# Kernel tuning notes

Hardware: AMD Instinct MI355X
Metric: run time of the kernel (lower is better)

The kernel has to match this reference:

```python
import jax, jax.numpy as jnp
import numpy as np

NUM_GRAPHS = 1024  # static number of segments for global_mean_pool


def setup_inputs() -> dict:
    key = jax.random.key(0)
    ks = jax.random.split(key, 16)
    N, E, F_IN, H = 100000, 1000000, 32, 64
    NUM_ATOM, NUM_ACT, L = 16, 8, 3
    s = 0.05
    x = jax.random.normal(ks[0], (N, F_IN), dtype=jnp.float32)
    edge_index = jax.random.randint(ks[1], (2, E), 0, N, dtype=jnp.int64)
    batch = jnp.sort(jax.random.randint(ks[2], (N,), 0, NUM_GRAPHS, dtype=jnp.int64))
    W_emb = jax.random.normal(ks[3], (F_IN, H), dtype=jnp.float32) * s
    b_emb = jnp.zeros((H,), dtype=jnp.float32)
    W_convs = jax.random.normal(ks[4], (L, H, H), dtype=jnp.float32) * s
    b_convs = jnp.zeros((L, H), dtype=jnp.float32)
    W_act = jax.random.normal(ks[5], (H, NUM_ACT), dtype=jnp.float32) * s
    b_act = jnp.zeros((NUM_ACT,), dtype=jnp.float32)
    W_tgt = jax.random.normal(ks[6], (H, 1), dtype=jnp.float32) * s
    b_tgt = jnp.zeros((1,), dtype=jnp.float32)
    W_atom = jax.random.normal(ks[7], (H, NUM_ATOM), dtype=jnp.float32) * s
    b_atom = jnp.zeros((NUM_ATOM,), dtype=jnp.float32)
    return {"x": x, "edge_index": edge_index, "batch": batch,
            "W_emb": W_emb, "b_emb": b_emb, "W_convs": W_convs, "b_convs": b_convs,
            "W_act": W_act, "b_act": b_act, "W_tgt": W_tgt, "b_tgt": b_tgt,
            "W_atom": W_atom, "b_atom": b_atom}


def reference(x, edge_index, batch, W_emb, b_emb, W_convs, b_convs,
              W_act, b_act, W_tgt, b_tgt, W_atom, b_atom):
    N = x.shape[0]
    # --- GCN normalization with self-loops (PyG GCNConv default) ---
    self_idx = jnp.arange(N, dtype=edge_index.dtype)
    src = jnp.concatenate([edge_index[0], self_idx])  # message source (row)
    dst = jnp.concatenate([edge_index[1], self_idx])  # aggregation target (col)
    ones_e = jnp.ones(src.shape[0], dtype=x.dtype)
    deg = jax.ops.segment_sum(ones_e, dst, num_segments=N)  # in-degree + self-loop
    dinv = jnp.where(deg > 0, jax.lax.rsqrt(deg), 0.0)
    norm = (dinv[src] * dinv[dst])[:, None]  # [E+N, 1]

    h = jax.nn.relu(x @ W_emb + b_emb)  # node embedding
    for i in range(W_convs.shape[0]):
        m = (h @ W_convs[i])[src] * norm            # gather + scale
        agg = jax.ops.segment_sum(m, dst, num_segments=N)  # scatter-add
        h = jax.nn.relu(agg + b_convs[i])

    # --- global mean pool over graphs ---
    cnt = jax.ops.segment_sum(jnp.ones(N, dtype=x.dtype), batch, num_segments=NUM_GRAPHS)
    pooled = jax.ops.segment_sum(h, batch, num_segments=NUM_GRAPHS)
    pooled = pooled / jnp.maximum(cnt, 1.0)[:, None]

    action_type_logits = pooled @ W_act + b_act            # [G, num_action_types]
    target_node_logits = (h @ W_tgt + b_tgt)[:, 0]         # [N]
    new_atom_type_logits = pooled @ W_atom + b_atom        # [G, num_atom_types]
    return (action_type_logits, target_node_logits, new_atom_type_logits, h)
```

## Files before the change

### kernel.cpp

```cpp
#include <hip/hip_runtime.h>
#include <hip/hip_fp16.h>

#define HD 64
#define FIN 32
#define NG 1024
#define STRIDE 64
#define SLOT0 4
#define DEGCAP 59
#define SH 72

#define BINW 128
#define NBMAX 1024
#define EPB 2048
#define BINCAP 2048

typedef _Float16 f16x8 __attribute__((ext_vector_type(8)));
typedef float f32x4 __attribute__((ext_vector_type(4)));
typedef int i32x4 __attribute__((ext_vector_type(4)));

__device__ __forceinline__ int fmap(int jt, int c) {
    return (jt < 2) ? (2 * c + jt) : (32 + 2 * c + (jt - 2));
}

__global__ __launch_bounds__(256) void k_prep(const int* __restrict__ dst,
                                              int* __restrict__ blkHist,
                                              int E, int NBINS,
                                              __half2* __restrict__ BaZR,
                                              __half2* __restrict__ BbZR,
                                              const float* __restrict__ Wconv,
                                              __half* __restrict__ Wf, int wtotal,
                                              const float* __restrict__ Wemb,
                                              __half* __restrict__ Wef) {
    __shared__ int hist[NBMAX];
    int b = blockIdx.x, t = threadIdx.x;
    if (b < 48) {
        int tid = b * 256 + t;
        if (tid < wtotal) {
            int layer = tid >> 12;
            int r = tid & 4095;
            int frag = r >> 9, lane = (r >> 3) & 63, e = r & 7;
            int jt = frag >> 1, kh = frag & 1;
            int k = kh * 32 + (lane >> 4) * 8 + e;
            int n = fmap(jt, lane & 15);
            Wf[tid] = (_Float16)Wconv[(size_t)layer * 4096 + k * 64 + n];
        }
    } else if (b < 56) {
        int tid = (b - 48) * 256 + t;
        if (tid < 2048) {
            int jt = tid >> 9, lane = (tid >> 3) & 63, e = tid & 7;
            int k = (lane >> 4) * 8 + e;
            int n = fmap(jt, lane & 15);
            Wef[tid] = (_Float16)Wemb[k * HD + n];
        }
    } else if (b == 56) {
        __half2 z = __floats2half2_rn(0.f, 0.f);
        if (t < 32) BaZR[t] = z;
        else if (t < 64) BbZR[t - 32] = z;
    }
    int e0 = b * EPB;
    if (e0 < E) {
        for (int i = t; i < NBMAX; i += 256) hist[i] = 0;
        __syncthreads();
        int e1 = e0 + EPB; if (e1 > E) e1 = E;
        for (int e = e0 + t; e < e1; e += 256) atomicAdd(&hist[dst[e] >> 7], 1);
        __syncthreads();
        for (int i = t; i < NBINS; i += 256) blkHist[b * NBMAX + i] = hist[i];
    }
}

__global__ __launch_bounds__(512) void k_scanA(int* __restrict__ blkHist,
                                               int* __restrict__ binTot, int nb) {
    __shared__ int s[512];
    int i = blockIdx.x;
    int t = threadIdx.x;
    int x = (t < nb) ? blkHist[t * NBMAX + i] : 0;
    s[t] = x;
    __syncthreads();
    for (int off = 1; off < 512; off <<= 1) {
        int v = s[t];
        int u = (t >= off) ? s[t - off] : 0;
        __syncthreads();
        s[t] = v + u;
        __syncthreads();
    }
    if (t < nb) blkHist[t * NBMAX + i] = s[t] - x;
    if (t == 511) binTot[i] = s[511];
}

__global__ __launch_bounds__(256) void k_scatter(const int* __restrict__ src,
                                                 const int* __restrict__ dst,
                                                 const int* __restrict__ blkBase,
                                                 int* __restrict__ binned,
                                                 int E, int NBINS) {
    __shared__ int base[NBMAX];
    __shared__ int lpos[NBMAX];
    int b = blockIdx.x, t = threadIdx.x;
    for (int i = t; i < NBMAX; i += 256) {
        lpos[i] = 0;
        base[i] = (i < NBINS) ? blkBase[b * NBMAX + i] : 0;
    }
    __syncthreads();
    int e0 = b * EPB;
    int e1 = e0 + EPB; if (e1 > E) e1 = E;
    for (int e = e0 + t; e < e1; e += 256) {
        int d = dst[e];
        int bin = d >> 7;
        int off = base[bin] + atomicAdd(&lpos[bin], 1);
        if (off < BINCAP)
            binned[bin * BINCAP + off] = (src[e] << 7) | (d & (BINW - 1));
    }
}

__global__ __launch_bounds__(256) void k_csr(const int* __restrict__ binned,
                                             const int* __restrict__ binTot,
                                             int* __restrict__ col, int N) {
    __shared__ int img[BINW * 64];
    __shared__ int cnt[BINW];
    int b = blockIdx.x, t = threadIdx.x;
    for (int i = t; i < BINW; i += 256) cnt[i] = 0;
    __syncthreads();
    int s = b * BINCAP;
    int tot = binTot[b]; if (tot > BINCAP) tot = BINCAP;
    int e = s + tot;
    for (int i = s + t; i < e; i += 256) {
        int w = binned[i];
        int ld = w & (BINW - 1);
        int p = atomicAdd(&cnt[ld], 1);
        if (p < STRIDE - SLOT0) img[ld * 64 + SLOT0 + p] = (int)((unsigned)w >> 7);
    }
    __syncthreads();
    for (int i = t; i < BINW; i += 256) img[i * 64] = cnt[i];
    __syncthreads();
    int v0 = b * BINW;
    int* out = col + ((size_t)v0 << 6);
    for (int j = t; j < BINW * 16; j += 256) {
        int row = j >> 4, j16 = j & 15;
        int node = v0 + row;
        int deg = cnt[row]; if (deg > DEGCAP) deg = DEGCAP;
        bool keep = (j16 == 0) || (j16 <= ((deg + 3) >> 2));
        if (node < N && keep)
            *(i32x4*)(out + j * 4) = *(i32x4*)&img[j * 4];
    }
}

__device__ __forceinline__ void gemm_from_lds(const __half* hs, const float* dvs,
                                              const float4* __restrict__ Wf4,
                                              __half2* __restrict__ Bout,
                                              int node0, int N, int t) {
    int lane = t & 63;
    int wv = t >> 6;
    int lm = lane & 15, kq = lane >> 4;
    union U { float4 f; f16x8 h; };
    U a0, a1;
    const __half* hrow = hs + (size_t)(wv * 16 + lm) * SH;
    a0.f = *(const float4*)(hrow + kq * 8);
    a1.f = *(const float4*)(hrow + 32 + kq * 8);
    f32x4 acc[4];
#pragma unroll
    for (int jt = 0; jt < 4; jt++) acc[jt] = (f32x4){0.f, 0.f, 0.f, 0.f};
#pragma unroll
    for (int jt = 0; jt < 4; jt++) {
        U b0, b1;
        b0.f = Wf4[(jt * 2 + 0) * 64 + lane];
        b1.f = Wf4[(jt * 2 + 1) * 64 + lane];
        acc[jt] = __builtin_amdgcn_mfma_f32_16x16x32_f16(a0.h, b0.h, acc[jt], 0, 0, 0);
        acc[jt] = __builtin_amdgcn_mfma_f32_16x16x32_f16(a1.h, b1.h, acc[jt], 0, 0, 0);
    }
#pragma unroll
    for (int r = 0; r < 4; r++) {
        int lv = wv * 16 + kq * 4 + r;
        int v = node0 + lv;
        if (v < N) {
            float dv = dvs[lv];
            *(Bout + (size_t)v * 32 + lm) = __floats2half2_rn(acc[0][r] * dv, acc[1][r] * dv);
            *(Bout + (size_t)v * 32 + 16 + lm) = __floats2half2_rn(acc[2][r] * dv, acc[3][r] * dv);
        }
    }
}

__global__ __launch_bounds__(256) void k_emb_gemm0(const float* __restrict__ x,
                                                   const float4* __restrict__ Wef4,
                                                   const float* __restrict__ bemb,
                                                   const int* __restrict__ col,
                                                   const float4* __restrict__ Wf0,
                                                   __half2* __restrict__ Bout, int N) {
    __shared__ __half hs[64 * SH];
    __shared__ float dvs[64];
    int t = threadIdx.x;
    int lane = t & 63;
    int wv = t >> 6;
    int node0 = blockIdx.x * 64;
    int nodew = node0 + wv * 16;
    int m = lane & 15, kq = lane >> 4;

    int vm = nodew + m;
    if (vm > N - 1) vm = N - 1;
    const float4* xr = (const float4*)(x + (size_t)vm * FIN + kq * 8);
    float4 xa = xr[0], xb = xr[1];
    f16x8 a;
    a[0] = (_Float16)xa.x; a[1] = (_Float16)xa.y; a[2] = (_Float16)xa.z; a[3] = (_Float16)xa.w;
    a[4] = (_Float16)xb.x; a[5] = (_Float16)xb.y; a[6] = (_Float16)xb.z; a[7] = (_Float16)xb.w;

    union U { float4 f; f16x8 h; };
    f32x4 acc[4];
#pragma unroll
    for (int jt = 0; jt < 4; jt++) {
        U b; b.f = Wef4[jt * 64 + lane];
        acc[jt] = (f32x4){0.f, 0.f, 0.f, 0.f};
        acc[jt] = __builtin_amdgcn_mfma_f32_16x16x32_f16(a, b.h, acc[jt], 0, 0, 0);
    }
    float b01x = bemb[2 * m], b01y = bemb[2 * m + 1];
    float b23x = bemb[32 + 2 * m], b23y = bemb[32 + 2 * m + 1];
    __half2 z = __floats2half2_rn(0.f, 0.f);
#pragma unroll
    for (int r = 0; r < 4; r++) {
        int lv = wv * 16 + kq * 4 + r;
        int v = node0 + lv;
        __half2 p01 = z, p23 = z;
        if (v < N) {
            p01 = __floats2half2_rn(fmaxf(acc[0][r] + b01x, 0.f),
                                    fmaxf(acc[1][r] + b01y, 0.f));
            p23 = __floats2half2_rn(fmaxf(acc[2][r] + b23x, 0.f),
                                    fmaxf(acc[3][r] + b23y, 0.f));
        }
        *(__half2*)(hs + (size_t)lv * SH + 2 * m) = p01;
        *(__half2*)(hs + (size_t)lv * SH + 32 + 2 * m) = p23;
        if (m == 0)
            dvs[lv] = (v < N) ? rsqrtf((float)(col[(size_t)v << 6] + 1)) : 1.f;
    }
    __syncthreads();
    gemm_from_lds(hs, dvs, Wf0, Bout, node0, N, t);
}

__global__ __launch_bounds__(256) void k_layer(const __half2* __restrict__ Bin,
                                               const int* __restrict__ col,
                                               const float* __restrict__ bias,
                                               const float4* __restrict__ Wnext,
                                               __half2* __restrict__ Bout,
                                               int N, int ZR) {
    __shared__ __half hs[64 * SH];
    __shared__ float dvs[64];
    int t = threadIdx.x;
    int lane = t & 63;
    int wv = t >> 6;
    int node0 = blockIdx.x * 64;
    int q = lane >> 4, p = lane & 15;
    float4 b4 = *(const float4*)(bias + 4 * p);

#pragma unroll
    for (int pass = 0; pass < 4; pass++) {
        int lv = wv * 16 + pass * 4 + q;
        int v = node0 + lv;
        int vc = (v < N) ? v : 0;
        const int* bucket = col + ((size_t)vc << 6);
        int degraw = bucket[0];
        int deg = degraw > DEGCAP ? DEGCAP : degraw;
        int rounds = (deg + 4) >> 2;

        float2 a0 = make_float2(0.f, 0.f), a1 = make_float2(0.f, 0.f);
        for (int rd = 0; rd < rounds; rd++) {
            int4 iq = *(const int4*)(bucket + SLOT0 + rd * 4);
            int idx[4] = {iq.x, iq.y, iq.z, iq.w};
#pragma unroll
            for (int r = 0; r < 4; r++) {
                int i = rd * 4 + r;
                idx[r] = (i < deg) ? idx[r] : ((i == deg) ? vc : ZR);
            }
            float2 raw[4];
#pragma unroll
            for (int r = 0; r < 4; r++)
                raw[r] = *(const float2*)(Bin + (size_t)idx[r] * 32 + p * 2);
#pragma unroll
            for (int r = 0; r < 4; r++) {
                float2 f0 = __half22float2(((const __half2*)&raw[r])[0]);
                float2 f1 = __half22float2(((const __half2*)&raw[r])[1]);
                a0.x += f0.x; a0.y += f0.y; a1.x += f1.x; a1.y += f1.y;
            }
        }
        float dv = rsqrtf((float)(degraw + 1));
        float r0 = fmaxf(dv * a0.x + b4.x, 0.f);
        float r1 = fmaxf(dv * a0.y + b4.y, 0.f);
        float r2 = fmaxf(dv * a1.x + b4.z, 0.f);
        float r3 = fmaxf(dv * a1.y + b4.w, 0.f);
        if (v >= N) { r0 = r1 = r2 = r3 = 0.f; dv = 1.f; }
        __half* hrow = hs + (size_t)lv * SH + 4 * p;
        *(__half2*)(hrow) = __floats2half2_rn(r0, r1);
        *(__half2*)(hrow + 2) = __floats2half2_rn(r2, r3);
        if (p == 0) dvs[lv] = dv;
    }
    __syncthreads();
    gemm_from_lds(hs, dvs, Wnext, Bout, node0, N, t);
}

__global__ __launch_bounds__(256) void k_gather_last(const __half2* __restrict__ Bin,
                                                     const int* __restrict__ col,
                                                     const float* __restrict__ bias,
                                                     float* __restrict__ hout,
                                                     const float* __restrict__ Wtgt,
                                                     const float* __restrict__ btgt,
                                                     float* __restrict__ tgt,
                                                     int N, int ZR) {
    int t = threadIdx.x;
    int lane = t & 63;
    int wv = t >> 6;
    int q = lane >> 4, p = lane & 15;
    int v = blockIdx.x * 16 + wv * 4 + q;
    if (v >= N) return;

    const int* bucket = col + ((size_t)v << 6);
    int degraw = bucket[0];
    int deg = degraw > DEGCAP ? DEGCAP : degraw;
    int rounds = (deg + 4) >> 2;

    float2 a0 = make_float2(0.f, 0.f), a1 = make_float2(0.f, 0.f);
    for (int rd = 0; rd < rounds; rd++) {
        int4 iq = *(const int4*)(bucket + SLOT0 + rd * 4);
        int idx[4] = {iq.x, iq.y, iq.z, iq.w};
#pragma unroll
        for (int r = 0; r < 4; r++) {
            int i = rd * 4 + r;
            idx[r] = (i < deg) ? idx[r] : ((i == deg) ? v : ZR);
        }
        float2 raw[4];
#pragma unroll
        for (int r = 0; r < 4; r++)
            raw[r] = *(const float2*)(Bin + (size_t)idx[r] * 32 + p * 2);
#pragma unroll
        for (int r = 0; r < 4; r++) {
            float2 f0 = __half22float2(((const __half2*)&raw[r])[0]);
            float2 f1 = __half22float2(((const __half2*)&raw[r])[1]);
            a0.x += f0.x; a0.y += f0.y; a1.x += f1.x; a1.y += f1.y;
        }
    }
    float dv = rsqrtf((float)(degraw + 1));
    float4 b4 = *(const float4*)(bias + 4 * p);
    float r0 = fmaxf(dv * a0.x + b4.x, 0.f);
    float r1 = fmaxf(dv * a0.y + b4.y, 0.f);
    float r2 = fmaxf(dv * a1.x + b4.z, 0.f);
    float r3 = fmaxf(dv * a1.y + b4.w, 0.f);
    *(f32x4*)(hout + (size_t)v * HD + 4 * p) = (f32x4){r0, r1, r2, r3};
    float4 w4 = *(const float4*)(Wtgt + 4 * p);
    float pp = r0 * w4.x + r1 * w4.y + r2 * w4.z + r3 * w4.w;
    pp += __shfl_xor(pp, 1, 64); pp += __shfl_xor(pp, 2, 64);
    pp += __shfl_xor(pp, 4, 64); pp += __shfl_xor(pp, 8, 64);
    if (p == 0) __builtin_nontemporal_store(pp + btgt[0], tgt + v);
}

__global__ __launch_bounds__(256) void k_pool(const float* __restrict__ h,
                                              const int* __restrict__ batch,
                                              const float* __restrict__ Wact,
                                              const float* __restrict__ bact,
                                              const float* __restrict__ Watom,
                                              const float* __restrict__ batom,
                                              float* __restrict__ out_act,
                                              float* __restrict__ out_atom, int N) {
    int g = blockIdx.x;
    int t = threadIdx.x;
    int q = t >> 4, p = t & 15;
    int lo = 0, hi = N;
    while (lo < hi) { int mid = (lo + hi) >> 1; if (batch[mid] < g) lo = mid + 1; else hi = mid; }
    int s = lo;
    hi = N;
    while (lo < hi) { int mid = (lo + hi) >> 1; if (batch[mid] < g + 1) lo = mid + 1; else hi = mid; }
    int e2 = lo;
    float4 acc = make_float4(0.f, 0.f, 0.f, 0.f);
    for (int v = s + q; v < e2; v += 16) {
        float4 c = *(const float4*)(h + (size_t)v * HD + p * 4);
        acc.x += c.x; acc.y += c.y; acc.z += c.z; acc.w += c.w;
    }
    __shared__ float4 part[16][16];
    part[q][p] = acc;
    __syncthreads();
    __shared__ float pl[HD];
    if (t < 16) {
        float4 tot = part[0][t];
#pragma unroll
        for (int k = 1; k < 16; k++) {
            float4 c = part[k][t];
            tot.x += c.x; tot.y += c.y; tot.z += c.z; tot.w += c.w;
        }
        float cnt = fmaxf((float)(e2 - s), 1.f);
        pl[t * 4 + 0] = tot.x / cnt; pl[t * 4 + 1] = tot.y / cnt;
        pl[t * 4 + 2] = tot.z / cnt; pl[t * 4 + 3] = tot.w / cnt;
    }
    __syncthreads();
    if (t < 8) {
        float a = bact[t];
#pragma unroll
        for (int k = 0; k < HD; k++) a += pl[k] * Wact[k * 8 + t];
        out_act[g * 8 + t] = a;
    }
    if (t < 16) {
        float a = batom[t];
#pragma unroll
        for (int k = 0; k < HD; k++) a += pl[k] * Watom[k * 16 + t];
        out_atom[g * 16 + t] = a;
    }
}

extern "C" void kernel_launch(void* const* d_in, const int* in_sizes, int n_in,
                              void* d_out, int out_size, void* d_ws, size_t ws_size,
                              hipStream_t stream) {
    const float* x     = (const float*)d_in[0];
    const int*   ei    = (const int*)d_in[1];
    const int*   batch = (const int*)d_in[2];
    const float* Wemb  = (const float*)d_in[3];
    const float* bemb  = (const float*)d_in[4];
    const float* Wconv = (const float*)d_in[5];
    const float* bconv = (const float*)d_in[6];
    const float* Wact  = (const float*)d_in[7];
    const float* bact  = (const float*)d_in[8];
    const float* Wtgt  = (const float*)d_in[9];
    const float* btgt  = (const float*)d_in[10];
    const float* Watom = (const float*)d_in[11];
    const float* batom = (const float*)d_in[12];

    const int N = in_sizes[0] / FIN;
    const int E = in_sizes[1] / 2;
    const int L = in_sizes[5] / (HD * HD);
    const int Npad = (N + 63) & ~63;
    const int ZR = Npad;

    int*     col = (int*)d_ws;
    __half2* Ba  = (__half2*)(col + ((size_t)N << 6));
    __half2* Bb  = Ba + (size_t)(Npad + 64) * 32;
    __half*  Wf  = (__half*)(Bb + (size_t)(Npad + 64) * 32);
    __half*  Wef = Wf + (size_t)L * 4096;

    int* binned  = (int*)Bb;
    int* blkHist = (int*)((char*)Bb + (8u << 20));
    int* binTot  = (int*)((char*)Bb + (11u << 20));

    const int* srcA = ei;
    const int* dstA = ei + E;

    float* out_act  = (float*)d_out;
    float* out_tgt  = out_act + (size_t)NG * 8;
    float* out_atom = out_tgt + N;
    float* out_h    = out_atom + (size_t)NG * 16;

    const int nbG = (N + 63) / 64;
    const int nbLast = (N + 15) / 16;
    const int wtotal = L * 4096;
    const int nbF1 = (E + EPB - 1) / EPB;
    const int NBINS = (N + BINW - 1) / BINW;
    const int nbPrep = nbF1 > 57 ? nbF1 : 57;

    k_prep<<<nbPrep, 256, 0, stream>>>(dstA, blkHist, E, NBINS,
                                       Ba + (size_t)ZR * 32, Bb + (size_t)ZR * 32,
                                       Wconv, Wf, wtotal, Wemb, Wef);
    k_scanA<<<NBINS, 512, 0, stream>>>(blkHist, binTot, nbF1);
    k_scatter<<<nbF1, 256, 0, stream>>>(srcA, dstA, blkHist, binned, E, NBINS);
    k_csr<<<NBINS, 256, 0, stream>>>(binned, binTot, col, N);
    k_emb_gemm0<<<nbG, 256, 0, stream>>>(x, (const float4*)Wef, bemb, col,
                                         (const float4*)Wf, Ba, N);

    __half2* cur = Ba;
    __half2* nxt = Bb;
    for (int l = 0; l < L - 1; ++l) {
        k_layer<<<nbG, 256, 0, stream>>>(cur, col, bconv + l * HD,
                                         (const float4*)(Wf + (size_t)(l + 1) * 4096),
                                         nxt, N, ZR);
        __half2* tmp = cur; cur = nxt; nxt = tmp;
    }
    k_gather_last<<<nbLast, 256, 0, stream>>>(cur, col, bconv + (size_t)(L - 1) * HD,
                                              out_h, Wtgt, btgt, out_tgt, N, ZR);
    k_pool<<<NG, 256, 0, stream>>>(out_h, batch, Wact, bact, Watom, batom,
                                   out_act, out_atom, N);
}
```

Measured before the change: 224.7 us.

## Fuse global mean-pool accumulation into last gather kernel via atomics

Moves the per-graph sum of final node features into the last gather kernel. Each block accumulates into shared memory per local graph and then does global atomic adds into a pooled buffer that the prep kernel zeroes. The pool kernel becomes a small heads kernel that only divides by the count and applies the two linear heads. This avoids re-reading the 25MB h output, in exchange for extra shared and global atomics and float summation order that is no longer deterministic.

```diff
diff --git a/kernel.cpp b/kernel.cpp
--- a/kernel.cpp
+++ b/kernel.cpp
@@ -30,7 +30,8 @@
                                               const float* __restrict__ Wconv,
                                               __half* __restrict__ Wf, int wtotal,
                                               const float* __restrict__ Wemb,
-                                              __half* __restrict__ Wef) {
+                                              __half* __restrict__ Wef,
+                                              float* __restrict__ pooled) {
     __shared__ int hist[NBMAX];
     int b = blockIdx.x, t = threadIdx.x;
     if (b < 48) {
@@ -56,6 +57,12 @@
         __half2 z = __floats2half2_rn(0.f, 0.f);
         if (t < 32) BaZR[t] = z;
         else if (t < 64) BbZR[t - 32] = z;
+    } else if (b < 61) {
+        f32x4* p4 = (f32x4*)pooled;
+        f32x4 z4 = (f32x4){0.f, 0.f, 0.f, 0.f};
+        int base = (b - 57) * 4096;
+#pragma unroll
+        for (int k = 0; k < 16; k++) p4[base + k * 256 + t] = z4;
     }
     int e0 = b * EPB;
     if (e0 < E) {
@@ -295,58 +302,90 @@
 __global__ __launch_bounds__(256) void k_gather_last(const __half2* __restrict__ Bin,
                                                      const int* __restrict__ col,
                                                      const float* __restrict__ bias,
+                                                     const int* __restrict__ batch,
+                                                     float* __restrict__ pooled,
                                                      float* __restrict__ hout,
                                                      const float* __restrict__ Wtgt,
                                                      const float* __restrict__ btgt,
                                                      float* __restrict__ tgt,
                                                      int N, int ZR) {
+    __shared__ float gsum[16 * HD];
     int t = threadIdx.x;
     int lane = t & 63;
     int wv = t >> 6;
     int q = lane >> 4, p = lane & 15;
-    int v = blockIdx.x * 16 + wv * 4 + q;
-    if (v >= N) return;
-
-    const int* bucket = col + ((size_t)v << 6);
-    int degraw = bucket[0];
-    int deg = degraw > DEGCAP ? DEGCAP : degraw;
-    int rounds = (deg + 4) >> 2;
-
-    float2 a0 = make_float2(0.f, 0.f), a1 = make_float2(0.f, 0.f);
-    for (int rd = 0; rd < rounds; rd++) {
-        int4 iq = *(const int4*)(bucket + SLOT0 + rd * 4);
-        int idx[4] = {iq.x, iq.y, iq.z, iq.w};
-#pragma unroll
-        for (int r = 0; r < 4; r++) {
-            int i = rd * 4 + r;
-            idx[r] = (i < deg) ? idx[r] : ((i == deg) ? v : ZR);
-        }
-        float2 raw[4];
-#pragma unroll
-        for (int r = 0; r < 4; r++)
-            raw[r] = *(const float2*)(Bin + (size_t)idx[r] * 32 + p * 2);
-#pragma unroll
-        for (int r = 0; r < 4; r++) {
-            float2 f0 = __half22float2(((const __half2*)&raw[r])[0]);
-            float2 f1 = __half22float2(((const __half2*)&raw[r])[1]);
-            a0.x += f0.x; a0.y += f0.y; a1.x += f1.x; a1.y += f1.y;
-        }
-    }
-    float dv = rsqrtf((float)(degraw + 1));
-    float4 b4 = *(const float4*)(bias + 4 * p);
-    float r0 = fmaxf(dv * a0.x + b4.x, 0.f);
-    float r1 = fmaxf(dv * a0.y + b4.y, 0.f);
-    float r2 = fmaxf(dv * a1.x + b4.z, 0.f);
-    float r3 = fmaxf(dv * a1.y + b4.w, 0.f);
-    *(f32x4*)(hout + (size_t)v * HD + 4 * p) = (f32x4){r0, r1, r2, r3};
-    float4 w4 = *(const float4*)(Wtgt + 4 * p);
-    float pp = r0 * w4.x + r1 * w4.y + r2 * w4.z + r3 * w4.w;
-    pp += __shfl_xor(pp, 1, 64); pp += __shfl_xor(pp, 2, 64);
-    pp += __shfl_xor(pp, 4, 64); pp += __shfl_xor(pp, 8, 64);
-    if (p == 0) __builtin_nontemporal_store(pp + btgt[0], tgt + v);
-}
-
-__global__ __launch_bounds__(256) void k_pool(const float* __restrict__ h,
+    int v0 = blockIdx.x * 16;
+    int v = v0 + wv * 4 + q;
+#pragma unroll
+    for (int k = 0; k < 4; k++) gsum[k * 256 + t] = 0.f;
+    int g0 = batch[(v0 < N) ? v0 : (N - 1)];
+    __syncthreads();
+
+    if (v < N) {
+        const int* bucket = col + ((size_t)v << 6);
+        int degraw = bucket[0];
+        int deg = degraw > DEGCAP ? DEGCAP : degraw;
+        int rounds = (deg + 4) >> 2;
+
+        float2 a0 = make_float2(0.f, 0.f), a1 = make_float2(0.f, 0.f);
+        for (int rd = 0; rd < rounds; rd++) {
+            int4 iq = *(const int4*)(bucket + SLOT0 + rd * 4);
+            int idx[4] = {iq.x, iq.y, iq.z, iq.w};
+#pragma unroll
+            for (int r = 0; r < 4; r++) {
+                int i = rd * 4 + r;
+                idx[r] = (i < deg) ? idx[r] : ((i == deg) ? v : ZR);
+            }
+            float2 raw[4];
+#pragma unroll
+            for (int r = 0; r < 4; r++)
+                raw[r] = *(const float2*)(Bin + (size_t)idx[r] * 32 + p * 2);
+#pragma unroll
+            for (int r = 0; r < 4; r++) {
+                float2 f0 = __half22float2(((const __half2*)&raw[r])[0]);
+                float2 f1 = __half22float2(((const __half2*)&raw[r])[1]);
+                a0.x += f0.x; a0.y += f0.y; a1.x += f1.x; a1.y += f1.y;
+            }
+        }
+        float dv = rsqrtf((float)(degraw + 1));
+        float4 b4 = *(const float4*)(bias + 4 * p);
+        float r0 = fmaxf(dv * a0.x + b4.x, 0.f);
+        float r1 = fmaxf(dv * a0.y + b4.y, 0.f);
+        float r2 = fmaxf(dv * a1.x + b4.z, 0.f);
+        float r3 = fmaxf(dv * a1.y + b4.w, 0.f);
+        *(f32x4*)(hout + (size_t)v * HD + 4 * p) = (f32x4){r0, r1, r2, r3};
+
+        int lg = batch[v] - g0;
+        if (lg < 16) {
+            atomicAdd(&gsum[lg * HD + 4 * p + 0], r0);
+            atomicAdd(&gsum[lg * HD + 4 * p + 1], r1);
+            atomicAdd(&gsum[lg * HD + 4 * p + 2], r2);
+            atomicAdd(&gsum[lg * HD + 4 * p + 3], r3);
+        } else {
+            atomicAdd(&pooled[(size_t)(g0 + lg) * HD + 4 * p + 0], r0);
+            atomicAdd(&pooled[(size_t)(g0 + lg) * HD + 4 * p + 1], r1);
+            atomicAdd(&pooled[(size_t)(g0 + lg) * HD + 4 * p + 2], r2);
+            atomicAdd(&pooled[(size_t)(g0 + lg) * HD + 4 * p + 3], r3);
+        }
+
+        float4 w4 = *(const float4*)(Wtgt + 4 * p);
+        float pp = r0 * w4.x + r1 * w4.y + r2 * w4.z + r3 * w4.w;
+        pp += __shfl_xor(pp, 1, 64); pp += __shfl_xor(pp, 2, 64);
+        pp += __shfl_xor(pp, 4, 64); pp += __shfl_xor(pp, 8, 64);
+        if (p == 0) __builtin_nontemporal_store(pp + btgt[0], tgt + v);
+    }
+    __syncthreads();
+
+    int vlast = v0 + 15; if (vlast > N - 1) vlast = N - 1;
+    int gspan = (v0 < N) ? (batch[vlast] - g0 + 1) : 0;
+    if (gspan > 16) gspan = 16;
+    for (int c = t; c < gspan * HD; c += 256) {
+        float s = gsum[c];
+        if (s != 0.f) atomicAdd(&pooled[(size_t)(g0 + (c >> 6)) * HD + (c & 63)], s);
+    }
+}
+
+__global__ __launch_bounds__(64) void k_heads(const float* __restrict__ pooled,
                                               const int* __restrict__ batch,
                                               const float* __restrict__ Wact,
                                               const float* __restrict__ bact,
@@ -356,45 +395,26 @@
                                               float* __restrict__ out_atom, int N) {
     int g = blockIdx.x;
     int t = threadIdx.x;
-    int q = t >> 4, p = t & 15;
     int lo = 0, hi = N;
     while (lo < hi) { int mid = (lo + hi) >> 1; if (batch[mid] < g) lo = mid + 1; else hi = mid; }
     int s = lo;
     hi = N;
     while (lo < hi) { int mid = (lo + hi) >> 1; if (batch[mid] < g + 1) lo = mid + 1; else hi = mid; }
-    int e2 = lo;
-    float4 acc = make_float4(0.f, 0.f, 0.f, 0.f);
-    for (int v = s + q; v < e2; v += 16) {
-        float4 c = *(const float4*)(h + (size_t)v * HD + p * 4);
-        acc.x += c.x; acc.y += c.y; acc.z += c.z; acc.w += c.w;
-    }
-    __shared__ float4 part[16][16];
-    part[q][p] = acc;
-    __syncthreads();
+    float cnt = fmaxf((float)(lo - s), 1.f);
     __shared__ float pl[HD];
-    if (t < 16) {
-        float4 tot = part[0][t];
-#pragma unroll
-        for (int k = 1; k < 16; k++) {
-            float4 c = part[k][t];
-            tot.x += c.x; tot.y += c.y; tot.z += c.z; tot.w += c.w;
-        }
-        float cnt = fmaxf((float)(e2 - s), 1.f);
-        pl[t * 4 + 0] = tot.x / cnt; pl[t * 4 + 1] = tot.y / cnt;
-        pl[t * 4 + 2] = tot.z / cnt; pl[t * 4 + 3] = tot.w / cnt;
-    }
+    pl[t] = pooled[(size_t)g * HD + t] / cnt;
     __syncthreads();
     if (t < 8) {
         float a = bact[t];
 #pragma unroll
         for (int k = 0; k < HD; k++) a += pl[k] * Wact[k * 8 + t];
         out_act[g * 8 + t] = a;
-    }
-    if (t < 16) {
-        float a = batom[t];
-#pragma unroll
-        for (int k = 0; k < HD; k++) a += pl[k] * Watom[k * 16 + t];
-        out_atom[g * 16 + t] = a;
+    } else if (t < 24) {
+        int j = t - 8;
+        float a = batom[j];
+#pragma unroll
+        for (int k = 0; k < HD; k++) a += pl[k] * Watom[k * 16 + j];
+        out_atom[g * 16 + j] = a;
     }
 }
 
@@ -426,6 +446,7 @@
     __half2* Bb  = Ba + (size_t)(Npad + 64) * 32;
     __half*  Wf  = (__half*)(Bb + (size_t)(Npad + 64) * 32);
     __half*  Wef = Wf + (size_t)L * 4096;
+    float*   pooled = (float*)(Wef + 2048);
 
     int* binned  = (int*)Bb;
     int* blkHist = (int*)((char*)Bb + (8u << 20));
@@ -444,11 +465,11 @@
     const int wtotal = L * 4096;
     const int nbF1 = (E + EPB - 1) / EPB;
     const int NBINS = (N + BINW - 1) / BINW;
-    const int nbPrep = nbF1 > 57 ? nbF1 : 57;
+    const int nbPrep = nbF1 > 61 ? nbF1 : 61;
 
     k_prep<<<nbPrep, 256, 0, stream>>>(dstA, blkHist, E, NBINS,
                                        Ba + (size_t)ZR * 32, Bb + (size_t)ZR * 32,
-                                       Wconv, Wf, wtotal, Wemb, Wef);
+                                       Wconv, Wf, wtotal, Wemb, Wef, pooled);
     k_scanA<<<NBINS, 512, 0, stream>>>(blkHist, binTot, nbF1);
     k_scatter<<<nbF1, 256, 0, stream>>>(srcA, dstA, blkHist, binned, E, NBINS);
     k_csr<<<NBINS, 256, 0, stream>>>(binned, binTot, col, N);
@@ -464,7 +485,8 @@
         __half2* tmp = cur; cur = nxt; nxt = tmp;
     }
     k_gather_last<<<nbLast, 256, 0, stream>>>(cur, col, bconv + (size_t)(L - 1) * HD,
+                                              batch, pooled,
                                               out_h, Wtgt, btgt, out_tgt, N, ZR);
-    k_pool<<<NG, 256, 0, stream>>>(out_h, batch, Wact, bact, Watom, batom,
+    k_heads<<<NG, 64, 0, stream>>>(pooled, batch, Wact, bact, Watom, batom,
                                    out_act, out_atom, N);
 }
```

Result: slower. 249.8 us (+11.1%).
